# Kernel tuning notes

Hardware: AMD Instinct MI355X
Metric: run time of the kernel (lower is better)

The kernel has to match this reference:

```python
import jax, jax.numpy as jnp
import numpy as np

WS = 9
PAD = WS // 2  # 4


def _unfold(x, H, W):
    # x: [N,C,H,W] -> [N,C,81,H,W], reflect-padded 9x9 windows,
    # tap order (row-major over kernel) matching torch F.unfold.
    xp = jnp.pad(x, ((0, 0), (0, 0), (PAD, PAD), (PAD, PAD)), mode='reflect')
    return jnp.stack(
        [xp[:, :, i:i + H, j:j + W] for i in range(WS) for j in range(WS)],
        axis=2,
    )


def _bilinear_align_corners(x, H, W):
    # torch F.interpolate(mode='bilinear', align_corners=True)
    N, C, h, w = x.shape
    ys = jnp.linspace(0.0, h - 1.0, H)
    xs = jnp.linspace(0.0, w - 1.0, W)
    y0 = jnp.floor(ys).astype(jnp.int32)
    x0 = jnp.floor(xs).astype(jnp.int32)
    y1 = jnp.minimum(y0 + 1, h - 1)
    x1 = jnp.minimum(x0 + 1, w - 1)
    wy = (ys - y0)[:, None]   # [H,1]
    wx = (xs - x0)[None, :]   # [1,W]
    g = lambda yi, xi: x[:, :, yi, :][:, :, :, xi]
    top = g(y0, x0) * (1.0 - wx) + g(y0, x1) * wx
    bot = g(y1, x0) * (1.0 - wx) + g(y1, x1) * wx
    return top * (1.0 - wy) + bot * wy


def setup_inputs() -> dict:
    key = jax.random.key(0)
    ks = jax.random.split(key, 6)
    N, H, W = 4, 128, 128
    return {
        'delta': jax.random.normal(ks[0], (N, 64, H, W), jnp.float32),
        'out': jax.random.normal(ks[1], (N, 2, H // 2, W // 2), jnp.float32),
        'ab_logits': jax.random.normal(ks[2], (N, 81, H * W), jnp.float32),
        'w1': jax.random.normal(ks[3], (16, 64), jnp.float32) * 0.125,
        'b1': jnp.zeros((16,), jnp.float32),
        'w2': jax.random.normal(ks[4], (16, 64), jnp.float32) * 0.125,
        'b2': jnp.zeros((16,), jnp.float32),
        'gamma_d': jnp.ones((), jnp.float32),
        'gamma_s': jnp.ones((), jnp.float32),
    }


def reference(delta, out, ab_logits, w1, b1, w2, b2, gamma_d, gamma_s):
    N, C, H, W = delta.shape
    # 1x1 convs
    f1 = jnp.einsum('nchw,oc->nohw', delta, w1) + b1[None, :, None, None]
    f2 = jnp.einsum('nchw,oc->nohw', delta, w2) + b2[None, :, None, None]
    # windowed squared-distance correlation
    f2_unf = _unfold(f2, H, W).reshape(N, 16, WS * WS, H * W)
    d_center = f1.reshape(N, 16, 1, H * W)
    delta_logits = -jnp.sum((d_center - f2_unf) ** 2, axis=1)  # [N,81,HW]
    attn = jax.nn.softmax(gamma_d * delta_logits + gamma_s * ab_logits, axis=1)
    # weighted local aggregation of (detached, upsampled) out
    out_up = _bilinear_align_corners(jax.lax.stop_gradient(out), H, W)
    out_unf = _unfold(out_up, H, W).reshape(N, 2, WS * WS, H * W)
    out_refine = jnp.sum(out_unf * attn[:, None], axis=2)  # [N,2,HW]
    return out_refine.reshape(N, 2, H, W)
```

## Files before the change

### kernel.cpp

```cpp
#include <hip/hip_runtime.h>

#define HGT 128
#define WID 128
#define HW  (HGT*WID)
#define CIN 64
#define NPIX (4*HW)
#define TS 16
#define HS 24
#define HPX (HS*HS)

__global__ __launch_bounds__(256) void pass1_kernel(
    const float* __restrict__ delta, const float* __restrict__ outlo,
    const float* __restrict__ w1, const float* __restrict__ b1,
    const float* __restrict__ w2, const float* __restrict__ b2,
    float4* __restrict__ f1p, float4* __restrict__ f2p, float4* __restrict__ rec)
{
    __shared__ float wlds[64][32];
    {
        const int t = threadIdx.x;
#pragma unroll
        for (int s = 0; s < 8; ++s) {
            const int idx = t + s * 256;
            const int c = idx >> 5, o = idx & 31;
            wlds[c][o] = (o < 16) ? w1[o * 64 + c] : w2[(o - 16) * 64 + c];
        }
    }
    __syncthreads();

    const int g = blockIdx.x * 256 + threadIdx.x;
    const int n = g >> 14;
    const int p = g & (HW - 1);

    float f1a[16], f2a[16];
#pragma unroll
    for (int o = 0; o < 16; ++o) { f1a[o] = b1[o]; f2a[o] = b2[o]; }

    const float* dbase = delta + n * CIN * HW + p;
#pragma unroll 4
    for (int c = 0; c < CIN; ++c) {
        const float d = dbase[c * HW];
        const float4* wr = (const float4*)(&wlds[c][0]);
#pragma unroll
        for (int k = 0; k < 4; ++k) {
            const float4 wv = wr[k];
            f1a[4*k+0] = fmaf(wv.x, d, f1a[4*k+0]);
            f1a[4*k+1] = fmaf(wv.y, d, f1a[4*k+1]);
            f1a[4*k+2] = fmaf(wv.z, d, f1a[4*k+2]);
            f1a[4*k+3] = fmaf(wv.w, d, f1a[4*k+3]);
        }
#pragma unroll
        for (int k = 0; k < 4; ++k) {
            const float4 wv = wr[4 + k];
            f2a[4*k+0] = fmaf(wv.x, d, f2a[4*k+0]);
            f2a[4*k+1] = fmaf(wv.y, d, f2a[4*k+1]);
            f2a[4*k+2] = fmaf(wv.z, d, f2a[4*k+2]);
            f2a[4*k+3] = fmaf(wv.w, d, f2a[4*k+3]);
        }
    }

    float f2sq = 0.f;
#pragma unroll
    for (int o = 0; o < 16; ++o) f2sq = fmaf(f2a[o], f2a[o], f2sq);

#pragma unroll
    for (int k = 0; k < 4; ++k) {
        f1p[k * NPIX + g] = make_float4(f1a[4*k], f1a[4*k+1], f1a[4*k+2], f1a[4*k+3]);
        f2p[k * NPIX + g] = make_float4(f2a[4*k], f2a[4*k+1], f2a[4*k+2], f2a[4*k+3]);
    }

    const int y = p >> 7, x = p & 127;
    const float ys = (float)(y * 63) / 127.0f;
    const float xs = (float)(x * 63) / 127.0f;
    const int iy0 = (int)ys, ix0 = (int)xs;
    const float fy = ys - (float)iy0, fx = xs - (float)ix0;
    const int iy1 = min(iy0 + 1, 63), ix1 = min(ix0 + 1, 63);
    const float* ob = outlo + n * 2 * 4096;
    float o01[2];
#pragma unroll
    for (int cc = 0; cc < 2; ++cc) {
        const float* oc = ob + cc * 4096;
        const float v00 = oc[iy0*64+ix0], v01 = oc[iy0*64+ix1];
        const float v10 = oc[iy1*64+ix0], v11 = oc[iy1*64+ix1];
        const float top = v00 + fx * (v01 - v00);
        const float bot = v10 + fx * (v11 - v10);
        o01[cc] = top + fy * (bot - top);
    }
    rec[g] = make_float4(o01[0], o01[1], f2sq, 0.f);
}

__global__ __launch_bounds__(256) void pass2_kernel(
    const float4* __restrict__ f1p, const float4* __restrict__ f2p,
    const float4* __restrict__ rec, const float* __restrict__ ab,
    const float* __restrict__ gdp, const float* __restrict__ gsp,
    float* __restrict__ outp)
{
    __shared__ float4 sf[5][HPX];

    const int t = threadIdx.x;
    const int n = blockIdx.z;
    const int bx = blockIdx.x * TS, by = blockIdx.y * TS;

#pragma unroll
    for (int s = 0; s < 3; ++s) {
        const int px = t + s * 256;
        if (px < HPX) {
            const int hy = px / 24, hx = px - hy * 24;
            int gy = by - 4 + hy; gy = gy < 0 ? -gy : (gy > 127 ? 254 - gy : gy);
            int gx = bx - 4 + hx; gx = gx < 0 ? -gx : (gx > 127 ? 254 - gx : gx);
            const int gp = n * HW + gy * 128 + gx;
            sf[0][px] = f2p[0 * NPIX + gp];
            sf[1][px] = f2p[1 * NPIX + gp];
            sf[2][px] = f2p[2 * NPIX + gp];
            sf[3][px] = f2p[3 * NPIX + gp];
            sf[4][px] = rec[gp];
        }
    }
    __syncthreads();

    const float gd = gdp[0], gs = gsp[0];
    const int tx = t & 15, ty = t >> 4;
    const int p = (by + ty) * 128 + (bx + tx);
    const int g = n * HW + p;

    float f1r[16];
#pragma unroll
    for (int k = 0; k < 4; ++k) {
        const float4 v = f1p[k * NPIX + g];
        f1r[4*k] = v.x; f1r[4*k+1] = v.y; f1r[4*k+2] = v.z; f1r[4*k+3] = v.w;
    }
    float f1sq = 0.f;
#pragma unroll
    for (int o = 0; o < 16; ++o) f1sq = fmaf(f1r[o], f1r[o], f1sq);
    const float c0 = -gd * f1sq;
    const float gd2 = 2.0f * gd;

    float s_ = 0.f, a0 = 0.f, a1 = 0.f;
    const float* abbase = ab + n * 81 * HW + p;

    for (int i = 0; i < 9; ++i) {
        const int hbase = (ty + i) * HS + tx;
        const float* abr = abbase + i * 9 * HW;
#pragma unroll
        for (int j = 0; j < 9; ++j) {
            const int h = hbase + j;
            const float4 A = sf[0][h], B = sf[1][h];
            const float4 C = sf[2][h], D = sf[3][h];
            float d0 = f1r[0]*A.x, d1 = f1r[1]*A.y, d2 = f1r[2]*A.z, d3 = f1r[3]*A.w;
            d0 = fmaf(f1r[ 4], B.x, d0); d1 = fmaf(f1r[ 5], B.y, d1);
            d2 = fmaf(f1r[ 6], B.z, d2); d3 = fmaf(f1r[ 7], B.w, d3);
            d0 = fmaf(f1r[ 8], C.x, d0); d1 = fmaf(f1r[ 9], C.y, d1);
            d2 = fmaf(f1r[10], C.z, d2); d3 = fmaf(f1r[11], C.w, d3);
            d0 = fmaf(f1r[12], D.x, d0); d1 = fmaf(f1r[13], D.y, d1);
            d2 = fmaf(f1r[14], D.z, d2); d3 = fmaf(f1r[15], D.w, d3);
            const float dot = (d0 + d1) + (d2 + d3);
            const float4 R = sf[4][h];
            float e = fmaf(-gd, R.z, fmaf(gd2, dot, c0));
            e = fmaf(gs, abr[j * HW], e);
            const float w = __expf(e);
            s_ += w;
            a0 = fmaf(w, R.x, a0);
            a1 = fmaf(w, R.y, a1);
        }
    }
    const float inv = 1.0f / s_;
    outp[(n * 2 + 0) * HW + p] = a0 * inv;
    outp[(n * 2 + 1) * HW + p] = a1 * inv;
}

extern "C" void kernel_launch(void* const* d_in, const int* in_sizes, int n_in,
                              void* d_out, int out_size, void* d_ws, size_t ws_size,
                              hipStream_t stream) {
    const float* delta = (const float*)d_in[0];
    const float* outlo = (const float*)d_in[1];
    const float* ab    = (const float*)d_in[2];
    const float* w1    = (const float*)d_in[3];
    const float* b1    = (const float*)d_in[4];
    const float* w2    = (const float*)d_in[5];
    const float* b2    = (const float*)d_in[6];
    const float* gd    = (const float*)d_in[7];
    const float* gs    = (const float*)d_in[8];
    float* outp = (float*)d_out;

    float4* f1p = (float4*)d_ws;
    float4* f2p = f1p + (size_t)4 * NPIX;
    float4* rec = f2p + (size_t)4 * NPIX;

    pass1_kernel<<<dim3(256), dim3(256), 0, stream>>>(delta, outlo, w1, b1, w2, b2,
                                                      f1p, f2p, rec);
    pass2_kernel<<<dim3(8, 8, 4), dim3(256), 0, stream>>>(f1p, f2p, rec, ab,
                                                          gd, gs, outp);
}
```

Measured before the change: 112.4 us.

## Compute two vertically adjacent pixels per thread and split window rows across thread halves

```diff
diff --git a/kernel.cpp b/kernel.cpp
--- a/kernel.cpp
+++ b/kernel.cpp
@@ -36,7 +36,7 @@
     for (int o = 0; o < 16; ++o) { f1a[o] = b1[o]; f2a[o] = b2[o]; }
 
     const float* dbase = delta + n * CIN * HW + p;
-#pragma unroll 4
+#pragma unroll 8
     for (int c = 0; c < CIN; ++c) {
         const float d = dbase[c * HW];
         const float4* wr = (const float4*)(&wlds[c][0]);
@@ -88,13 +88,26 @@
     rec[g] = make_float4(o01[0], o01[1], f2sq, 0.f);
 }
 
-__global__ __launch_bounds__(256) void pass2_kernel(
+#define DOT16(fr, A, B, C, D, out)                                             \
+    {                                                                          \
+        float d0 = fr[0]*A.x, d1 = fr[1]*A.y, d2 = fr[2]*A.z, d3 = fr[3]*A.w;  \
+        d0 = fmaf(fr[ 4], B.x, d0); d1 = fmaf(fr[ 5], B.y, d1);                \
+        d2 = fmaf(fr[ 6], B.z, d2); d3 = fmaf(fr[ 7], B.w, d3);                \
+        d0 = fmaf(fr[ 8], C.x, d0); d1 = fmaf(fr[ 9], C.y, d1);                \
+        d2 = fmaf(fr[10], C.z, d2); d3 = fmaf(fr[11], C.w, d3);                \
+        d0 = fmaf(fr[12], D.x, d0); d1 = fmaf(fr[13], D.y, d1);                \
+        d2 = fmaf(fr[14], D.z, d2); d3 = fmaf(fr[15], D.w, d3);                \
+        out = (d0 + d1) + (d2 + d3);                                           \
+    }
+
+__global__ __launch_bounds__(256, 1) void pass2_kernel(
     const float4* __restrict__ f1p, const float4* __restrict__ f2p,
     const float4* __restrict__ rec, const float* __restrict__ ab,
     const float* __restrict__ gdp, const float* __restrict__ gsp,
     float* __restrict__ outp)
 {
     __shared__ float4 sf[5][HPX];
+    __shared__ float part[6][128];
 
     const int t = threadIdx.x;
     const int n = blockIdx.z;
@@ -118,53 +131,85 @@
     __syncthreads();
 
     const float gd = gdp[0], gs = gsp[0];
-    const int tx = t & 15, ty = t >> 4;
-    const int p = (by + ty) * 128 + (bx + tx);
-    const int g = n * HW + p;
-
-    float f1r[16];
+    const int tx   = t & 15;
+    const int ty2  = (t >> 4) & 7;
+    const int half = t >> 7;
+    const int y0 = ty2 * 2;
+    const int p0 = (by + y0) * 128 + (bx + tx);
+    const int g0 = n * HW + p0;
+
+    float f1r0[16], f1r1[16];
 #pragma unroll
     for (int k = 0; k < 4; ++k) {
-        const float4 v = f1p[k * NPIX + g];
-        f1r[4*k] = v.x; f1r[4*k+1] = v.y; f1r[4*k+2] = v.z; f1r[4*k+3] = v.w;
-    }
-    float f1sq = 0.f;
-#pragma unroll
-    for (int o = 0; o < 16; ++o) f1sq = fmaf(f1r[o], f1r[o], f1sq);
-    const float c0 = -gd * f1sq;
+        const float4 v0 = f1p[k * NPIX + g0];
+        f1r0[4*k] = v0.x; f1r0[4*k+1] = v0.y; f1r0[4*k+2] = v0.z; f1r0[4*k+3] = v0.w;
+        const float4 v1 = f1p[k * NPIX + g0 + 128];
+        f1r1[4*k] = v1.x; f1r1[4*k+1] = v1.y; f1r1[4*k+2] = v1.z; f1r1[4*k+3] = v1.w;
+    }
+    float f1sq0 = 0.f, f1sq1 = 0.f;
+#pragma unroll
+    for (int o = 0; o < 16; ++o) {
+        f1sq0 = fmaf(f1r0[o], f1r0[o], f1sq0);
+        f1sq1 = fmaf(f1r1[o], f1r1[o], f1sq1);
+    }
+    const float c00 = -gd * f1sq0, c01 = -gd * f1sq1;
     const float gd2 = 2.0f * gd;
 
-    float s_ = 0.f, a0 = 0.f, a1 = 0.f;
-    const float* abbase = ab + n * 81 * HW + p;
-
-    for (int i = 0; i < 9; ++i) {
-        const int hbase = (ty + i) * HS + tx;
-        const float* abr = abbase + i * 9 * HW;
+    float s0 = 0.f, a00 = 0.f, a01 = 0.f;
+    float s1 = 0.f, a10 = 0.f, a11 = 0.f;
+    const float* ab0 = ab + n * 81 * HW + p0;
+
+    for (int q = 0; q < 5; ++q) {
+        const int ii = half * 5 + q;
+        const int hbase = (y0 + ii) * HS + tx;
+        const float* abr0 = ab0 + ii * 9 * HW;
+        const float* abr1 = ab0 + 128 + (ii - 1) * 9 * HW;
+        const bool do0 = (ii < 9);
+        const bool do1 = (ii > 0);
 #pragma unroll
         for (int j = 0; j < 9; ++j) {
             const int h = hbase + j;
             const float4 A = sf[0][h], B = sf[1][h];
             const float4 C = sf[2][h], D = sf[3][h];
-            float d0 = f1r[0]*A.x, d1 = f1r[1]*A.y, d2 = f1r[2]*A.z, d3 = f1r[3]*A.w;
-            d0 = fmaf(f1r[ 4], B.x, d0); d1 = fmaf(f1r[ 5], B.y, d1);
-            d2 = fmaf(f1r[ 6], B.z, d2); d3 = fmaf(f1r[ 7], B.w, d3);
-            d0 = fmaf(f1r[ 8], C.x, d0); d1 = fmaf(f1r[ 9], C.y, d1);
-            d2 = fmaf(f1r[10], C.z, d2); d3 = fmaf(f1r[11], C.w, d3);
-            d0 = fmaf(f1r[12], D.x, d0); d1 = fmaf(f1r[13], D.y, d1);
-            d2 = fmaf(f1r[14], D.z, d2); d3 = fmaf(f1r[15], D.w, d3);
-            const float dot = (d0 + d1) + (d2 + d3);
             const float4 R = sf[4][h];
-            float e = fmaf(-gd, R.z, fmaf(gd2, dot, c0));
-            e = fmaf(gs, abr[j * HW], e);
-            const float w = __expf(e);
-            s_ += w;
-            a0 = fmaf(w, R.x, a0);
-            a1 = fmaf(w, R.y, a1);
-        }
-    }
-    const float inv = 1.0f / s_;
-    outp[(n * 2 + 0) * HW + p] = a0 * inv;
-    outp[(n * 2 + 1) * HW + p] = a1 * inv;
+            if (do0) {
+                float dot;
+                DOT16(f1r0, A, B, C, D, dot);
+                float e = fmaf(-gd, R.z, fmaf(gd2, dot, c00));
+                e = fmaf(gs, abr0[j * HW], e);
+                const float w = __expf(e);
+                s0 += w;
+                a00 = fmaf(w, R.x, a00);
+                a01 = fmaf(w, R.y, a01);
+            }
+            if (do1) {
+                float dot;
+                DOT16(f1r1, A, B, C, D, dot);
+                float e = fmaf(-gd, R.z, fmaf(gd2, dot, c01));
+                e = fmaf(gs, abr1[j * HW], e);
+                const float w = __expf(e);
+                s1 += w;
+                a10 = fmaf(w, R.x, a10);
+                a11 = fmaf(w, R.y, a11);
+            }
+        }
+    }
+
+    const int tb = t & 127;
+    if (half == 1) {
+        part[0][tb] = s0; part[1][tb] = a00; part[2][tb] = a01;
+        part[3][tb] = s1; part[4][tb] = a10; part[5][tb] = a11;
+    }
+    __syncthreads();
+    if (half == 0) {
+        s0 += part[0][tb]; a00 += part[1][tb]; a01 += part[2][tb];
+        s1 += part[3][tb]; a10 += part[4][tb]; a11 += part[5][tb];
+        const float i0 = 1.0f / s0, i1 = 1.0f / s1;
+        outp[(n * 2 + 0) * HW + p0]       = a00 * i0;
+        outp[(n * 2 + 1) * HW + p0]       = a01 * i0;
+        outp[(n * 2 + 0) * HW + p0 + 128] = a10 * i1;
+        outp[(n * 2 + 1) * HW + p0 + 128] = a11 * i1;
+    }
 }
 
 extern "C" void kernel_launch(void* const* d_in, const int* in_sizes, int n_in,
```

Result: slower. 126.1 us (+12.2%).

## Split 81 window taps across four thread groups per pixel in pass2

Applied to the files above, without the earlier changes.

```diff
diff --git a/kernel.cpp b/kernel.cpp
--- a/kernel.cpp
+++ b/kernel.cpp
@@ -36,7 +36,7 @@
     for (int o = 0; o < 16; ++o) { f1a[o] = b1[o]; f2a[o] = b2[o]; }
 
     const float* dbase = delta + n * CIN * HW + p;
-#pragma unroll 4
+#pragma unroll 8
     for (int c = 0; c < CIN; ++c) {
         const float d = dbase[c * HW];
         const float4* wr = (const float4*)(&wlds[c][0]);
@@ -88,37 +88,63 @@
     rec[g] = make_float4(o01[0], o01[1], f2sq, 0.f);
 }
 
-__global__ __launch_bounds__(256) void pass2_kernel(
+#define DOT16(fr, A, B, C, D, out)                                             \
+    {                                                                          \
+        float d0 = fr[0]*A.x, d1 = fr[1]*A.y, d2 = fr[2]*A.z, d3 = fr[3]*A.w;  \
+        d0 = fmaf(fr[ 4], B.x, d0); d1 = fmaf(fr[ 5], B.y, d1);                \
+        d2 = fmaf(fr[ 6], B.z, d2); d3 = fmaf(fr[ 7], B.w, d3);                \
+        d0 = fmaf(fr[ 8], C.x, d0); d1 = fmaf(fr[ 9], C.y, d1);                \
+        d2 = fmaf(fr[10], C.z, d2); d3 = fmaf(fr[11], C.w, d3);                \
+        d0 = fmaf(fr[12], D.x, d0); d1 = fmaf(fr[13], D.y, d1);                \
+        d2 = fmaf(fr[14], D.z, d2); d3 = fmaf(fr[15], D.w, d3);                \
+        out = (d0 + d1) + (d2 + d3);                                           \
+    }
+
+#define TAP(h, av)                                                             \
+    {                                                                          \
+        const float4 A = sf[0][h], B = sf[1][h];                               \
+        const float4 C = sf[2][h], D = sf[3][h];                               \
+        float dot;                                                             \
+        DOT16(f1r, A, B, C, D, dot);                                           \
+        const float4 R = sf[4][h];                                             \
+        float e = fmaf(-gd, R.z, fmaf(gd2, dot, c0));                          \
+        e = fmaf(gs, (av), e);                                                 \
+        const float w = __expf(e);                                             \
+        s_ += w;                                                               \
+        a0 = fmaf(w, R.x, a0);                                                 \
+        a1 = fmaf(w, R.y, a1);                                                 \
+    }
+
+__global__ __launch_bounds__(1024, 4) void pass2_kernel(
     const float4* __restrict__ f1p, const float4* __restrict__ f2p,
     const float4* __restrict__ rec, const float* __restrict__ ab,
     const float* __restrict__ gdp, const float* __restrict__ gsp,
     float* __restrict__ outp)
 {
     __shared__ float4 sf[5][HPX];
+    __shared__ float part[3][3][256];
 
     const int t = threadIdx.x;
     const int n = blockIdx.z;
     const int bx = blockIdx.x * TS, by = blockIdx.y * TS;
 
-#pragma unroll
-    for (int s = 0; s < 3; ++s) {
-        const int px = t + s * 256;
-        if (px < HPX) {
-            const int hy = px / 24, hx = px - hy * 24;
-            int gy = by - 4 + hy; gy = gy < 0 ? -gy : (gy > 127 ? 254 - gy : gy);
-            int gx = bx - 4 + hx; gx = gx < 0 ? -gx : (gx > 127 ? 254 - gx : gx);
-            const int gp = n * HW + gy * 128 + gx;
-            sf[0][px] = f2p[0 * NPIX + gp];
-            sf[1][px] = f2p[1 * NPIX + gp];
-            sf[2][px] = f2p[2 * NPIX + gp];
-            sf[3][px] = f2p[3 * NPIX + gp];
-            sf[4][px] = rec[gp];
-        }
+    if (t < HPX) {
+        const int hy = t / 24, hx = t - hy * 24;
+        int gy = by - 4 + hy; gy = gy < 0 ? -gy : (gy > 127 ? 254 - gy : gy);
+        int gx = bx - 4 + hx; gx = gx < 0 ? -gx : (gx > 127 ? 254 - gx : gx);
+        const int gp = n * HW + gy * 128 + gx;
+        sf[0][t] = f2p[0 * NPIX + gp];
+        sf[1][t] = f2p[1 * NPIX + gp];
+        sf[2][t] = f2p[2 * NPIX + gp];
+        sf[3][t] = f2p[3 * NPIX + gp];
+        sf[4][t] = rec[gp];
     }
     __syncthreads();
 
     const float gd = gdp[0], gs = gsp[0];
-    const int tx = t & 15, ty = t >> 4;
+    const int px = t & 255;
+    const int q  = t >> 8;
+    const int tx = px & 15, ty = px >> 4;
     const int p = (by + ty) * 128 + (bx + tx);
     const int g = n * HW + p;
 
@@ -135,36 +161,42 @@
     const float gd2 = 2.0f * gd;
 
     float s_ = 0.f, a0 = 0.f, a1 = 0.f;
-    const float* abbase = ab + n * 81 * HW + p;
-
-    for (int i = 0; i < 9; ++i) {
-        const int hbase = (ty + i) * HS + tx;
-        const float* abr = abbase + i * 9 * HW;
-#pragma unroll
-        for (int j = 0; j < 9; ++j) {
-            const int h = hbase + j;
-            const float4 A = sf[0][h], B = sf[1][h];
-            const float4 C = sf[2][h], D = sf[3][h];
-            float d0 = f1r[0]*A.x, d1 = f1r[1]*A.y, d2 = f1r[2]*A.z, d3 = f1r[3]*A.w;
-            d0 = fmaf(f1r[ 4], B.x, d0); d1 = fmaf(f1r[ 5], B.y, d1);
-            d2 = fmaf(f1r[ 6], B.z, d2); d3 = fmaf(f1r[ 7], B.w, d3);
-            d0 = fmaf(f1r[ 8], C.x, d0); d1 = fmaf(f1r[ 9], C.y, d1);
-            d2 = fmaf(f1r[10], C.z, d2); d3 = fmaf(f1r[11], C.w, d3);
-            d0 = fmaf(f1r[12], D.x, d0); d1 = fmaf(f1r[13], D.y, d1);
-            d2 = fmaf(f1r[14], D.z, d2); d3 = fmaf(f1r[15], D.w, d3);
-            const float dot = (d0 + d1) + (d2 + d3);
-            const float4 R = sf[4][h];
-            float e = fmaf(-gd, R.z, fmaf(gd2, dot, c0));
-            e = fmaf(gs, abr[j * HW], e);
-            const float w = __expf(e);
-            s_ += w;
-            a0 = fmaf(w, R.x, a0);
-            a1 = fmaf(w, R.y, a1);
-        }
-    }
-    const float inv = 1.0f / s_;
-    outp[(n * 2 + 0) * HW + p] = a0 * inv;
-    outp[(n * 2 + 1) * HW + p] = a1 * inv;
+
+    const float* abp = ab + (size_t)n * 81 * HW + p + (size_t)q * HW;
+    int jj = q;
+    int h  = ty * HS + tx + q;
+#pragma unroll 2
+    for (int it = 0; it < 20; ++it) {
+        TAP(h, abp[0]);
+        abp += 4 * HW;
+        jj += 4;
+        const bool carry = (jj >= 9);
+        jj -= carry ? 9 : 0;
+        h  += carry ? 19 : 4;
+    }
+    if (q == 3) {
+        const int h80 = (ty + 8) * HS + tx + 8;
+        const float* ab80 = ab + (size_t)n * 81 * HW + p + (size_t)80 * HW;
+        TAP(h80, ab80[0]);
+    }
+
+    if (q > 0) {
+        part[q - 1][0][px] = s_;
+        part[q - 1][1][px] = a0;
+        part[q - 1][2][px] = a1;
+    }
+    __syncthreads();
+    if (q == 0) {
+#pragma unroll
+        for (int k = 0; k < 3; ++k) {
+            s_ += part[k][0][px];
+            a0 += part[k][1][px];
+            a1 += part[k][2][px];
+        }
+        const float inv = 1.0f / s_;
+        outp[(n * 2 + 0) * HW + p] = a0 * inv;
+        outp[(n * 2 + 1) * HW + p] = a1 * inv;
+    }
 }
 
 extern "C" void kernel_launch(void* const* d_in, const int* in_sizes, int n_in,
@@ -187,6 +219,6 @@
 
     pass1_kernel<<<dim3(256), dim3(256), 0, stream>>>(delta, outlo, w1, b1, w2, b2,
                                                       f1p, f2p, rec);
-    pass2_kernel<<<dim3(8, 8, 4), dim3(256), 0, stream>>>(f1p, f2p, rec, ab,
-                                                          gd, gs, outp);
+    pass2_kernel<<<dim3(8, 8, 4), dim3(1024), 0, stream>>>(f1p, f2p, rec, ab,
+                                                           gd, gs, outp);
 }
```

After: 107.1 us. -4.7%, faster.
